# Optimization experiments

Hardware: AMD Instinct MI355X
Metric: run time of the kernel (lower is better)

## Reference

```python
import jax, jax.numpy as jnp
import numpy as np

B, L, D, H, M = 2, 4096, 1024, 16, 256
DH = D // H
EPS = 1e-6
LN_EPS = 1e-5


def setup_inputs() -> dict:
    key = jax.random.key(0)
    ks = jax.random.split(key, 6)
    inp = {
        "x": jax.random.normal(ks[0], (B, L, D), jnp.float32),
        "Wq": jax.random.normal(ks[1], (D, D), jnp.float32) * (D ** -0.5),
        "Wk": jax.random.normal(ks[2], (D, D), jnp.float32) * (D ** -0.5),
        "Wv": jax.random.normal(ks[3], (D, D), jnp.float32) * (D ** -0.5),
        "Wo": jax.random.normal(ks[4], (D, D), jnp.float32) * (D ** -0.5),
        "proj": jax.random.normal(ks[5], (H, M, DH), jnp.float32),
        "ln_g": jnp.ones((D,), jnp.float32),
        "ln_b": jnp.zeros((D,), jnp.float32),
        "scale_factor": 2,
    }
    return inp


def _heads(t, W):
    b, l, _ = t.shape
    return (t @ W).reshape(b, l, H, DH).transpose(0, 2, 1, 3)  # bhld


def _favor_features(u, proj):
    # u: [B,H,L,DH] already scaled by d_head**-0.25; proj: [H,M,DH]
    dash = jnp.einsum("bhld,hmd->bhlm", u, proj)
    diag = 0.5 * jnp.sum(u * u, axis=-1, keepdims=True)  # [B,H,L,1]
    stab = jnp.max(dash, axis=-1, keepdims=True)
    return jnp.exp(dash - diag - stab) * (M ** -0.5)  # [B,H,L,M]


def reference(x, Wq, Wk, Wv, Wo, proj, ln_g, ln_b, scale_factor):
    b, l, d = x.shape
    # nearest-neighbor upsample along sequence (F.interpolate default mode)
    up = jnp.repeat(x, scale_factor, axis=1)  # [B, L*s, D]

    scale = DH ** -0.25
    q = _heads(up, Wq) * scale   # [B,H,Lq,DH]
    k = _heads(x, Wk) * scale    # [B,H,L,DH]
    v = _heads(x, Wv)            # [B,H,L,DH]

    qf = _favor_features(q, proj)  # [B,H,Lq,M]
    kf = _favor_features(k, proj)  # [B,H,L,M]

    kv = jnp.einsum("bhlm,bhld->bhmd", kf, v)          # [B,H,M,DH]
    k_sum = jnp.sum(kf, axis=2)                          # [B,H,M]
    z = 1.0 / (jnp.einsum("bhlm,bhm->bhl", qf, k_sum) + EPS)
    attn = jnp.einsum("bhlm,bhmd->bhld", qf, kv) * z[..., None]

    lq = attn.shape[2]
    y = attn.transpose(0, 2, 1, 3).reshape(b, lq, d) @ Wo
    y = jax.nn.gelu(y, approximate=False)

    mu = jnp.mean(y, axis=-1, keepdims=True)
    var = jnp.mean((y - mu) ** 2, axis=-1, keepdims=True)
    return (y - mu) * jax.lax.rsqrt(var + LN_EPS) * ln_g + ln_b
```

## Files before the change

kernel.cpp:

```cpp
#include <hip/hip_runtime.h>

static constexpr int kB  = 2;
static constexpr int kL  = 4096;
static constexpr int kD  = 1024;
static constexpr int kH  = 16;
static constexpr int kDH = 64;
static constexpr int kM  = 256;
static constexpr int kN  = kB * kL;
static constexpr float kScale    = 0.35355339059327373f;
static constexpr float kInvSqrtM = 0.0625f;
static constexpr float kEps   = 1e-6f;
static constexpr float kLnEps = 1e-5f;

typedef __attribute__((ext_vector_type(8))) short short8;
typedef __attribute__((ext_vector_type(4))) float f32x4;

__device__ __forceinline__ float bf2f(unsigned short h) {
  union { unsigned int u; float f; } c;
  c.u = ((unsigned int)h) << 16;
  return c.f;
}
__device__ __forceinline__ unsigned short f2bf(float f) {
  union { float f; unsigned int u; } c;
  c.f = f;
  unsigned int u = c.u;
  u += 0x7fffu + ((u >> 16) & 1u);
  return (unsigned short)(u >> 16);
}

__device__ __forceinline__ void gload_lds16(const unsigned short* g,
                                            unsigned short* l) {
  __builtin_amdgcn_global_load_lds(
      (const __attribute__((address_space(1))) unsigned int*)g,
      (__attribute__((address_space(3))) unsigned int*)l, 16, 0, 0);
}

__device__ __forceinline__ void xcd_swizzle(int& bx, int& by) {
  const int nwg = gridDim.x * gridDim.y;
  const int bid = blockIdx.x + gridDim.x * blockIdx.y;
  const int cpx = nwg >> 3;
  const int sb  = (bid & 7) * cpx + (bid >> 3);
  bx = sb % gridDim.x;
  by = sb / gridDim.x;
}

__global__ __launch_bounds__(256) void cast_bf16_kernel(
    const float* __restrict__ in, unsigned short* __restrict__ out)
{
  const int i = blockIdx.x * 256 + threadIdx.x;
  float4 v = ((const float4*)in)[i];
  ushort4 o;
  o.x = f2bf(v.x); o.y = f2bf(v.y); o.z = f2bf(v.z); o.w = f2bf(v.w);
  ((ushort4*)out)[i] = o;
}

__global__ __launch_bounds__(256) void transpose_cast4_kernel(
    const float* __restrict__ W0, const float* __restrict__ W1,
    const float* __restrict__ W2, const float* __restrict__ W3,
    unsigned short* __restrict__ WqkvT, unsigned short* __restrict__ WoT)
{
  __shared__ float tile[32][33];
  const int z = blockIdx.z;
  const float* W = (z == 0) ? W0 : (z == 1) ? W1 : (z == 2) ? W2 : W3;
  unsigned short* WT = (z < 3) ? (WqkvT + (size_t)z * kD * kD) : WoT;
  const int n0 = blockIdx.x * 32, k0 = blockIdx.y * 32;
  const int t = threadIdx.x, kk = t >> 5, nn = t & 31;
#pragma unroll
  for (int i = 0; i < 4; ++i)
    tile[kk + i * 8][nn] = W[(size_t)(k0 + kk + i * 8) * kD + n0 + nn];
  __syncthreads();
#pragma unroll
  for (int i = 0; i < 4; ++i)
    WT[(size_t)(n0 + kk + i * 8) * kD + k0 + nn] = f2bf(tile[nn][kk + i * 8]);
}

#define GEMM_BK64_BODY(Aptr, Bptr, arow0, bcol0)                              \
  const int lrow = lane >> 3;                                                 \
  const int lcol = ((lane & 7) ^ lrow) * 8;        \
  f32x4 acc[4][4];                                                            \
  _Pragma("unroll")                                                           \
  for (int i = 0; i < 4; ++i)                                                 \
    _Pragma("unroll")                                                         \
    for (int j = 0; j < 4; ++j) acc[i][j] = (f32x4)0.f;                       \
  for (int k0 = 0; k0 < kD; k0 += 64) {                                       \
    _Pragma("unroll")                                                         \
    for (int i = 0; i < 4; ++i) {                                             \
      const int r0 = w * 32 + i * 8;                                          \
      gload_lds16(&Aptr[(size_t)(arow0 + r0 + lrow) * kD + k0 + lcol],        \
                  &As[r0 * 64]);                                              \
      gload_lds16(&Bptr[(size_t)(bcol0 + r0 + lrow) * kD + k0 + lcol],        \
                  &Bs[r0 * 64]);                                              \
    }                                                                         \
    __syncthreads();                                                          \
    _Pragma("unroll")                                                         \
    for (int ks = 0; ks < 2; ++ks) {                                          \
      short8 av[4], bv[4];                                                    \
      const int ch = ks * 4 + q;                                              \
      _Pragma("unroll")                                                       \
      for (int i = 0; i < 4; ++i)                                             \
        av[i] = *(const short8*)&As[(wr + i * 16 + c) * 64 +                  \
                                    ((ch ^ (c & 7)) * 8)];                    \
      _Pragma("unroll")                                                       \
      for (int j = 0; j < 4; ++j)                                             \
        bv[j] = *(const short8*)&Bs[(wc + j * 16 + c) * 64 +                  \
                                    ((ch ^ (c & 7)) * 8)];                    \
      _Pragma("unroll")                                                       \
      for (int i = 0; i < 4; ++i)                                             \
        _Pragma("unroll")                                                     \
        for (int j = 0; j < 4; ++j)                                           \
          acc[i][j] = __builtin_amdgcn_mfma_f32_16x16x32_bf16(                \
              av[i], bv[j], acc[i][j], 0, 0, 0);                              \
    }                                                                         \
    __syncthreads();                                                          \
  }

__global__ __launch_bounds__(256) void gemm_qk_mfma(
    const unsigned short* __restrict__ A, const unsigned short* __restrict__ BT,
    unsigned short* __restrict__ Qb, unsigned short* __restrict__ Kb)
{
  __shared__ unsigned short As[128 * 64];
  __shared__ unsigned short Bs[128 * 64];
  const int tid = threadIdx.x, lane = tid & 63, w = tid >> 6;
  const int q = lane >> 4, c = lane & 15;
  const int wr = (w >> 1) * 64, wc = (w & 1) * 64;
  int bx, by; xcd_swizzle(bx, by);
  const int row0 = by * 128, col0 = bx * 128;

  GEMM_BK64_BODY(A, BT, row0, col0)

  unsigned short* O = (col0 < 1024) ? Qb : Kb;
  const int cl0 = col0 & 1023;
#pragma unroll
  for (int i = 0; i < 4; ++i)
#pragma unroll
    for (int j = 0; j < 4; ++j)
#pragma unroll
      for (int r = 0; r < 4; ++r) {
        const int row = row0 + wr + i * 16 + q * 4 + r;
        const int col = cl0 + wc + j * 16 + c;
        O[(size_t)row * kD + col] = f2bf(kScale * acc[i][j][r]);
      }
}

__global__ __launch_bounds__(256) void gemm_vt_mfma(
    const unsigned short* __restrict__ A, const unsigned short* __restrict__ BT,
    unsigned short* __restrict__ VT)
{
  __shared__ unsigned short As[128 * 64];
  __shared__ unsigned short Bs[128 * 64];
  const int tid = threadIdx.x, lane = tid & 63, w = tid >> 6;
  const int q = lane >> 4, c = lane & 15;
  const int wr = (w >> 1) * 64, wc = (w & 1) * 64;
  int bx, by; xcd_swizzle(bx, by);
  const int row0 = bx * 128, col0 = by * 128;

  GEMM_BK64_BODY(A, BT, row0, col0)

#pragma unroll
  for (int i = 0; i < 4; ++i)
#pragma unroll
    for (int j = 0; j < 4; ++j)
#pragma unroll
      for (int r = 0; r < 4; ++r) {
        const int row = row0 + wr + i * 16 + q * 4 + r;
        const int col = col0 + wc + j * 16 + c;
        const int bq = col >> 12, l = col & 4095;
        const int h = row >> 6, d = row & 63;
        VT[((size_t)((bq * 16 + h) * 64 + d)) * (size_t)kL + l] =
            f2bf(acc[i][j][r]);
      }
}

__global__ __launch_bounds__(256) void gemm_wo_mfma(
    const unsigned short* __restrict__ A, const unsigned short* __restrict__ BT,
    unsigned short* __restrict__ Yb)
{
  __shared__ unsigned short As[128 * 64];
  __shared__ unsigned short Bs[128 * 64];
  const int tid = threadIdx.x, lane = tid & 63, w = tid >> 6;
  const int q = lane >> 4, c = lane & 15;
  const int wr = (w >> 1) * 64, wc = (w & 1) * 64;
  int bx, by; xcd_swizzle(bx, by);
  const int row0 = by * 128, col0 = bx * 128;

  GEMM_BK64_BODY(A, BT, row0, col0)

#pragma unroll
  for (int i = 0; i < 4; ++i)
#pragma unroll
    for (int j = 0; j < 4; ++j)
#pragma unroll
      for (int r = 0; r < 4; ++r) {
        const int row = row0 + wr + i * 16 + q * 4 + r;
        const int col = col0 + wc + j * 16 + c;
        Yb[(size_t)row * kD + col] = f2bf(acc[i][j][r]);
      }
}

__global__ __launch_bounds__(256) void favor_k_mfma(
    const unsigned short* __restrict__ U, const unsigned short* __restrict__ projb,
    unsigned short* __restrict__ F)
{
  __shared__ unsigned short Us[128 * 72];
  __shared__ unsigned short Ps[256 * 72];
  __shared__ float diagp[256];
  __shared__ float diag[128];
  unsigned short* Tbuf = Us;
  const int bh = blockIdx.x, b = bh >> 4, h = bh & 15;
  const int l0 = blockIdx.y * 128;
  const int tid = threadIdx.x, lane = tid & 63, w = tid >> 6;
  const int q = lane >> 4, c = lane & 15;
  const int wr = w * 32;

#pragma unroll
  for (int it = 0; it < 4; ++it) {
    int idx = it * 256 + tid;
    int row = idx >> 3, col8 = idx & 7;
    *(uint4*)&Us[row * 72 + col8 * 8] =
        *(const uint4*)&U[((size_t)(b * kL + l0 + row)) * kD + h * kDH + col8 * 8];
  }
#pragma unroll
  for (int it = 0; it < 8; ++it) {
    int idx = it * 256 + tid;
    int row = idx >> 3, col8 = idx & 7;
    *(uint4*)&Ps[row * 72 + col8 * 8] =
        *(const uint4*)&projb[((size_t)(h * kM + row)) * kDH + col8 * 8];
  }
  __syncthreads();

  {
    int row = tid & 127, half = tid >> 7;
    const unsigned short* ur = &Us[row * 72 + half * 32];
    float s = 0.f;
#pragma unroll
    for (int d8 = 0; d8 < 4; ++d8) {
      uint4 raw = *(const uint4*)&ur[d8 * 8];
      const unsigned short* us = (const unsigned short*)&raw;
#pragma unroll
      for (int j = 0; j < 8; ++j) { float v = bf2f(us[j]); s = fmaf(v, v, s); }
    }
    diagp[half * 128 + row] = s;
  }

  f32x4 acc[2][16];
#pragma unroll
  for (int i = 0; i < 2; ++i)
#pragma unroll
    for (int j = 0; j < 16; ++j) acc[i][j] = (f32x4)0.f;

#pragma unroll
  for (int ks = 0; ks < 2; ++ks) {
    short8 av[2];
#pragma unroll
    for (int i = 0; i < 2; ++i)
      av[i] = *(const short8*)&Us[(wr + i * 16 + c) * 72 + ks * 32 + q * 8];
#pragma unroll
    for (int jb = 0; jb < 2; ++jb) {
      short8 bv[8];
#pragma unroll
      for (int jl = 0; jl < 8; ++jl)
        bv[jl] = *(const short8*)&Ps[((jb * 8 + jl) * 16 + c) * 72 + ks * 32 + q * 8];
#pragma unroll
      for (int jl = 0; jl < 8; ++jl)
#pragma unroll
        for (int i = 0; i < 2; ++i)
          acc[i][jb * 8 + jl] = __builtin_amdgcn_mfma_f32_16x16x32_bf16(
              av[i], bv[jl], acc[i][jb * 8 + jl], 0, 0, 0);
    }
  }

  __syncthreads();
  if (tid < 128) diag[tid] = 0.5f * (diagp[tid] + diagp[128 + tid]);
  __syncthreads();

#pragma unroll
  for (int i = 0; i < 2; ++i)
#pragma unroll
    for (int r = 0; r < 4; ++r) {
      const int lrow = wr + i * 16 + q * 4 + r;
      float mx = -3.4e38f;
#pragma unroll
      for (int j = 0; j < 16; ++j) mx = fmaxf(mx, acc[i][j][r]);
      mx = fmaxf(mx, __shfl_xor(mx, 1, 64));
      mx = fmaxf(mx, __shfl_xor(mx, 2, 64));
      mx = fmaxf(mx, __shfl_xor(mx, 4, 64));
      mx = fmaxf(mx, __shfl_xor(mx, 8, 64));
      const float base = diag[lrow] + mx;
#pragma unroll
      for (int j = 0; j < 16; ++j)
        acc[i][j][r] = __expf(acc[i][j][r] - base) * kInvSqrtM;
    }

#pragma unroll
  for (int mc = 0; mc < 4; ++mc) {
    __syncthreads();
#pragma unroll
    for (int jl = 0; jl < 4; ++jl) {
      const int jj = mc * 4 + jl;
#pragma unroll
      for (int i = 0; i < 2; ++i) {
        ushort4 o;
        o.x = f2bf(acc[i][jj][0]); o.y = f2bf(acc[i][jj][1]);
        o.z = f2bf(acc[i][jj][2]); o.w = f2bf(acc[i][jj][3]);
        *(ushort4*)&Tbuf[(jl * 16 + c) * 136 + wr + i * 16 + q * 4] = o;
      }
    }
    __syncthreads();
#pragma unroll
    for (int it = 0; it < 4; ++it) {
      int idx = it * 256 + tid;
      int row = idx >> 4, col8 = idx & 15;
      *(uint4*)&F[((size_t)(bh * kM + mc * 64 + row)) * (size_t)kL +
                  l0 + col8 * 8] = *(const uint4*)&Tbuf[row * 136 + col8 * 8];
    }
  }
}

__global__ __launch_bounds__(256) void fused_qf_attn(
    const unsigned short* __restrict__ U, const unsigned short* __restrict__ projb,
    const unsigned short* __restrict__ KVT, unsigned short* __restrict__ ATTN)
{
  __shared__ unsigned short SA[22016];
  __shared__ float diagp[256];
  __shared__ float diag[128];
  __shared__ unsigned short ksumS[256];
  unsigned short* Us  = SA;
  unsigned short* Ps2 = SA + 9216;
  unsigned short* kvs = SA;
  unsigned short* qs  = SA + 16896;
  const int bh = blockIdx.x, b = bh >> 4, h = bh & 15;
  const int l0 = blockIdx.y * 128;
  const int tid = threadIdx.x, lane = tid & 63, w = tid >> 6;
  const int q = lane >> 4, c = lane & 15;
  const int wr = w * 32;

#pragma unroll
  for (int it = 0; it < 4; ++it) {
    int idx = it * 256 + tid;
    int row = idx >> 3, col8 = idx & 7;
    *(uint4*)&Us[row * 72 + col8 * 8] =
        *(const uint4*)&U[((size_t)(b * kL + l0 + row)) * kD + h * kDH + col8 * 8];
  }
#pragma unroll
  for (int it = 0; it < 4; ++it) {
    int idx = it * 256 + tid;
    int row = idx >> 3, col8 = idx & 7;
    *(uint4*)&Ps2[row * 72 + col8 * 8] =
        *(const uint4*)&projb[((size_t)(h * kM + row)) * kDH + col8 * 8];
  }
  __syncthreads();

  {
    int row = tid & 127, half = tid >> 7;
    const unsigned short* ur = &Us[row * 72 + half * 32];
    float s = 0.f;
#pragma unroll
    for (int d8 = 0; d8 < 4; ++d8) {
      uint4 raw = *(const uint4*)&ur[d8 * 8];
      const unsigned short* us = (const unsigned short*)&raw;
#pragma unroll
      for (int j = 0; j < 8; ++j) { float v = bf2f(us[j]); s = fmaf(v, v, s); }
    }
    diagp[half * 128 + row] = s;
  }

  f32x4 acc[2][16];
#pragma unroll
  for (int i = 0; i < 2; ++i)
#pragma unroll
    for (int j = 0; j < 16; ++j) acc[i][j] = (f32x4)0.f;

#pragma unroll
  for (int half = 0; half < 2; ++half) {
    if (half == 1) {
      __syncthreads();
#pragma unroll
      for (int it = 0; it < 4; ++it) {
        int idx = it * 256 + tid;
        int row = idx >> 3, col8 = idx & 7;
        *(uint4*)&Ps2[row * 72 + col8 * 8] =
            *(const uint4*)&projb[((size_t)(h * kM + 128 + row)) * kDH + col8 * 8];
      }
      __syncthreads();
    }
#pragma unroll
    for (int ks = 0; ks < 2; ++ks) {
      short8 av[2];
#pragma unroll
      for (int i = 0; i < 2; ++i)
        av[i] = *(const short8*)&Us[(wr + i * 16 + c) * 72 + ks * 32 + q * 8];
      short8 bv[8];
#pragma unroll
      for (int jl = 0; jl < 8; ++jl)
        bv[jl] = *(const short8*)&Ps2[(jl * 16 + c) * 72 + ks * 32 + q * 8];
#pragma unroll
      for (int jl = 0; jl < 8; ++jl)
#pragma unroll
        for (int i = 0; i < 2; ++i)
          acc[i][half * 8 + jl] = __builtin_amdgcn_mfma_f32_16x16x32_bf16(
              av[i], bv[jl], acc[i][half * 8 + jl], 0, 0, 0);
    }
  }

  __syncthreads();
  if (tid < 128) diag[tid] = 0.5f * (diagp[tid] + diagp[128 + tid]);
#pragma unroll
  for (int it = 0; it < 8; ++it) {
    int idx = it * 256 + tid;
    int row = idx >> 5, col8 = (idx & 31) * 8;
    *(uint4*)&kvs[row * 264 + col8] =
        *(const uint4*)&KVT[(size_t)bh * (80 * kM) + row * kM + col8];
  }
  if (tid < 32)
    *(uint4*)&ksumS[tid * 8] =
        *(const uint4*)&KVT[(size_t)bh * (80 * kM) + 64 * kM + tid * 8];
  __syncthreads();

#pragma unroll
  for (int i = 0; i < 2; ++i)
#pragma unroll
    for (int r = 0; r < 4; ++r) {
      const int lrow = wr + i * 16 + q * 4 + r;
      float mx = -3.4e38f;
#pragma unroll
      for (int j = 0; j < 16; ++j) mx = fmaxf(mx, acc[i][j][r]);
      mx = fmaxf(mx, __shfl_xor(mx, 1, 64));
      mx = fmaxf(mx, __shfl_xor(mx, 2, 64));
      mx = fmaxf(mx, __shfl_xor(mx, 4, 64));
      mx = fmaxf(mx, __shfl_xor(mx, 8, 64));
      const float base = diag[lrow] + mx;
#pragma unroll
      for (int j = 0; j < 16; ++j)
        acc[i][j][r] = __expf(acc[i][j][r] - base) * kInvSqrtM;
    }

  float z_[2][4];
#pragma unroll
  for (int i = 0; i < 2; ++i)
#pragma unroll
    for (int r = 0; r < 4; ++r) {
      float d = 0.f;
#pragma unroll
      for (int j = 0; j < 16; ++j)
        d = fmaf(acc[i][j][r], bf2f(ksumS[j * 16 + c]), d);
      d += __shfl_xor(d, 1, 64);
      d += __shfl_xor(d, 2, 64);
      d += __shfl_xor(d, 4, 64);
      d += __shfl_xor(d, 8, 64);
      z_[i][r] = 1.f / (d + kEps);
    }

  f32x4 acc2[2][4];
#pragma unroll
  for (int i = 0; i < 2; ++i)
#pragma unroll
    for (int j = 0; j < 4; ++j) acc2[i][j] = (f32x4)0.f;

#pragma unroll
  for (int kk = 0; kk < 8; ++kk) {
#pragma unroll
    for (int i = 0; i < 2; ++i)
#pragma unroll
      for (int jj2 = 0; jj2 < 2; ++jj2) {
        const int jj = kk * 2 + jj2;
#pragma unroll
        for (int r = 0; r < 4; ++r)
          qs[(wr + i * 16 + q * 4 + r) * 40 + jj2 * 16 + c] =
              f2bf(acc[i][jj][r]);
      }
    __syncthreads();
    short8 bv2[4];
#pragma unroll
    for (int j = 0; j < 4; ++j)
      bv2[j] = *(const short8*)&kvs[(j * 16 + c) * 264 + kk * 32 + q * 8];
#pragma unroll
    for (int i = 0; i < 2; ++i) {
      short8 av2 = *(const short8*)&qs[(w * 32 + i * 16 + c) * 40 + q * 8];
#pragma unroll
      for (int j = 0; j < 4; ++j)
        acc2[i][j] = __builtin_amdgcn_mfma_f32_16x16x32_bf16(
            av2, bv2[j], acc2[i][j], 0, 0, 0);
    }
    __syncthreads();
  }

#pragma unroll
  for (int i = 0; i < 2; ++i)
#pragma unroll
    for (int r = 0; r < 4; ++r) {
      const int row = l0 + w * 32 + i * 16 + q * 4 + r;
      const size_t base = ((size_t)(b * kL + row)) * kD + h * kDH;
#pragma unroll
      for (int j = 0; j < 4; ++j)
        ATTN[base + j * 16 + c] = f2bf(acc2[i][j][r] * z_[i][r]);
    }
}

__global__ __launch_bounds__(256) void kv_mfma(
    const unsigned short* __restrict__ KFT, const unsigned short* __restrict__ VT,
    float* __restrict__ KVP, float* __restrict__ KSP)
{
  __shared__ unsigned short As[128 * 32];
  __shared__ unsigned short Bs[64 * 32];
  const int bh = blockIdx.x, mtile = blockIdx.y, split = blockIdx.z;
  const int tid = threadIdx.x, lane = tid & 63, w = tid >> 6;
  const int q = lane >> 4, c = lane & 15;
  const int l0 = split * 512;
  const unsigned short* Abase = KFT + ((size_t)(bh * kM + mtile * 128)) * kL + l0;
  const unsigned short* Bbase = VT + ((size_t)(bh * kDH)) * kL + l0;
  const int lrow = lane >> 2, lcol = (lane & 3) * 8;

  f32x4 acc[2][4];
#pragma unroll
  for (int i = 0; i < 2; ++i)
#pragma unroll
    for (int j = 0; j < 4; ++j) acc[i][j] = (f32x4)0.f;
  float ksr[2] = {0.f, 0.f};

  for (int k0 = 0; k0 < 512; k0 += 32) {
#pragma unroll
    for (int i = 0; i < 2; ++i) {
      const int r0 = w * 32 + i * 16;
      gload_lds16(&Abase[(size_t)(r0 + lrow) * kL + k0 + lcol], &As[r0 * 32]);
    }
    gload_lds16(&Bbase[(size_t)(w * 16 + lrow) * kL + k0 + lcol], &Bs[w * 16 * 32]);
    __syncthreads();
    short8 av[2], bv[4];
#pragma unroll
    for (int i = 0; i < 2; ++i) {
      av[i] = *(const short8*)&As[(w * 32 + i * 16 + c) * 32 + q * 8];
#pragma unroll
      for (int e = 0; e < 8; ++e) ksr[i] += bf2f((unsigned short)av[i][e]);
    }
#pragma unroll
    for (int j = 0; j < 4; ++j)
      bv[j] = *(const short8*)&Bs[(j * 16 + c) * 32 + q * 8];
#pragma unroll
    for (int i = 0; i < 2; ++i)
#pragma unroll
      for (int j = 0; j < 4; ++j)
        acc[i][j] = __builtin_amdgcn_mfma_f32_16x16x32_bf16(
            av[i], bv[j], acc[i][j], 0, 0, 0);
    __syncthreads();
  }

  const int blk = (bh * 2 + mtile) * 8 + split;
  float* op = KVP + (size_t)blk * (128 * 64);
#pragma unroll
  for (int i = 0; i < 2; ++i)
#pragma unroll
    for (int j = 0; j < 4; ++j)
#pragma unroll
      for (int r = 0; r < 4; ++r)
        op[(w * 32 + i * 16 + q * 4 + r) * 64 + j * 16 + c] = acc[i][j][r];

#pragma unroll
  for (int i = 0; i < 2; ++i) {
    float s = ksr[i];
    s += __shfl_xor(s, 16, 64);
    s += __shfl_xor(s, 32, 64);
    if (q == 0) KSP[blk * 128 + w * 32 + i * 16 + c] = s;
  }
}

__global__ __launch_bounds__(256) void kv_reduce_kernel(
    const float* __restrict__ KVP, const float* __restrict__ KSP,
    unsigned short* __restrict__ KVT)
{
  const int blk = blockIdx.x;
  const int bh = blk / 80, n = blk - bh * 80;
  const int t = threadIdx.x;
  const int mt = t >> 7, ml = t & 127;
  float s = 0.f;
  if (n < 64) {
#pragma unroll
    for (int sp = 0; sp < 8; ++sp)
      s += KVP[((size_t)((bh * 2 + mt) * 8 + sp)) * (128 * 64) + ml * 64 + n];
  } else if (n == 64) {
#pragma unroll
    for (int sp = 0; sp < 8; ++sp)
      s += KSP[((bh * 2 + mt) * 8 + sp) * 128 + ml];
  }
  KVT[(size_t)bh * (80 * kM) + n * kM + t] = f2bf(s);
}

__global__ __launch_bounds__(256) void gelu_ln_kernel(
    const unsigned short* __restrict__ Yb, const float* __restrict__ lng,
    const float* __restrict__ lnb, float* __restrict__ OUT)
{
  __shared__ float r1[4], r2[4];
  const int n = blockIdx.x;
  const int tid = threadIdx.x, lane = tid & 63, w = tid >> 6;

  ushort4 yv = ((const ushort4*)(Yb + (size_t)n * kD))[tid];
  float y0 = bf2f(yv.x), y1 = bf2f(yv.y), y2 = bf2f(yv.z), y3 = bf2f(yv.w);
  float g0 = 0.5f * y0 * (1.f + erff(y0 * 0.70710678118654752f));
  float g1 = 0.5f * y1 * (1.f + erff(y1 * 0.70710678118654752f));
  float g2 = 0.5f * y2 * (1.f + erff(y2 * 0.70710678118654752f));
  float g3 = 0.5f * y3 * (1.f + erff(y3 * 0.70710678118654752f));

  float s  = (g0 + g1) + (g2 + g3);
  float ss = (g0 * g0 + g1 * g1) + (g2 * g2 + g3 * g3);
#pragma unroll
  for (int off = 32; off; off >>= 1) {
    s  += __shfl_xor(s, off, 64);
    ss += __shfl_xor(ss, off, 64);
  }
  if (lane == 0) { r1[w] = s; r2[w] = ss; }
  __syncthreads();
  s  = (r1[0] + r1[1]) + (r1[2] + r1[3]);
  ss = (r2[0] + r2[1]) + (r2[2] + r2[3]);
  float mu  = s * (1.f / (float)kD);
  float var = ss * (1.f / (float)kD) - mu * mu;
  float inv = rsqrtf(var + kLnEps);

  float4 gg = ((const float4*)lng)[tid];
  float4 bb = ((const float4*)lnb)[tid];
  float4 o;
  o.x = (g0 - mu) * inv * gg.x + bb.x;
  o.y = (g1 - mu) * inv * gg.y + bb.y;
  o.z = (g2 - mu) * inv * gg.z + bb.z;
  o.w = (g3 - mu) * inv * gg.w + bb.w;

  const int b = n >> 12, l = n & 4095;
  const int cc = tid * 4;
  size_t base = ((size_t)(b * 8192 + 2 * l)) * kD + cc;
  *(float4*)(OUT + base)      = o;
  *(float4*)(OUT + base + kD) = o;
}

extern "C" void kernel_launch(void* const* d_in, const int* in_sizes, int n_in,
                              void* d_out, int out_size, void* d_ws, size_t ws_size,
                              hipStream_t stream)
{
  (void)in_sizes; (void)n_in; (void)out_size; (void)ws_size;
  const float* x    = (const float*)d_in[0];
  const float* Wq   = (const float*)d_in[1];
  const float* Wk   = (const float*)d_in[2];
  const float* Wv   = (const float*)d_in[3];
  const float* Wo   = (const float*)d_in[4];
  const float* proj = (const float*)d_in[5];
  const float* lng  = (const float*)d_in[6];
  const float* lnb  = (const float*)d_in[7];
  float* out = (float*)d_out;

  char* ws = (char*)d_ws;
  const size_t MB = 1024 * 1024;
  unsigned short* xb    = (unsigned short*)(ws);
  unsigned short* WqkvT = (unsigned short*)(ws + 16 * MB);
  unsigned short* WoT   = (unsigned short*)(ws + 22 * MB);
  unsigned short* Qb    = (unsigned short*)(ws + 24 * MB);
  unsigned short* Kb    = (unsigned short*)(ws + 40 * MB);
  unsigned short* VT    = (unsigned short*)(ws + 56 * MB);
  float* KVP            = (float*)(ws + 72 * MB);
  unsigned short* KFT   = (unsigned short*)(ws + 136 * MB);
  float* KSP            = (float*)(ws + 200 * MB);
  unsigned short* KVT   = (unsigned short*)(ws + 201 * MB);
  unsigned short* projb = (unsigned short*)(ws + 203 * MB);
  unsigned short* ATTN  = Kb;
  unsigned short* Yb    = (unsigned short*)(ws + 72 * MB);
  unsigned short* WvT   = WqkvT + (size_t)2 * kD * kD;

  cast_bf16_kernel<<<(kN * kD) / 1024, 256, 0, stream>>>(x, xb);
  cast_bf16_kernel<<<(kH * kM * kDH) / 1024, 256, 0, stream>>>(proj, projb);
  transpose_cast4_kernel<<<dim3(32, 32, 4), 256, 0, stream>>>(
      Wq, Wk, Wv, Wo, WqkvT, WoT);

  gemm_qk_mfma<<<dim3(16, 64), 256, 0, stream>>>(xb, WqkvT, Qb, Kb);
  gemm_vt_mfma<<<dim3(8, 64), 256, 0, stream>>>(WvT, xb, VT);

  favor_k_mfma<<<dim3(32, 32), 256, 0, stream>>>(Kb, projb, KFT);
  kv_mfma<<<dim3(32, 2, 8), 256, 0, stream>>>(KFT, VT, KVP, KSP);
  kv_reduce_kernel<<<32 * 80, 256, 0, stream>>>(KVP, KSP, KVT);

  fused_qf_attn<<<dim3(32, 32), 256, 0, stream>>>(Qb, projb, KVT, ATTN);

  gemm_wo_mfma<<<dim3(8, 64), 256, 0, stream>>>(ATTN, WoT, Yb);

  gelu_ln_kernel<<<kN, 256, 0, stream>>>(Yb, lng, lnb, out);
}
```

Before: 329.1 us.

## Merge QK and V projection GEMMs into one launch; widen kv_mfma K-tile to 64

The separate Q/K and V^T projection GEMMs are combined into a single launch of 24x64 blocks. Blocks with bx>=16 compute the V^T tile by swapping operands, which removes one launch and its tail. Separately, kv_mfma now stages 64-wide K chunks with an XOR swizzle on the LDS layout. That halves its loop iterations and barriers and is meant to reduce LDS bank conflicts. In exchange it doubles shared memory per block, and the xcd_swizzle mapping over the larger grid may change cache locality.

```diff
diff --git a/kernel.cpp b/kernel.cpp
--- a/kernel.cpp
+++ b/kernel.cpp
@@ -114,9 +114,10 @@
     __syncthreads();                                                          \
   }
 
-__global__ __launch_bounds__(256) void gemm_qk_mfma(
-    const unsigned short* __restrict__ A, const unsigned short* __restrict__ BT,
-    unsigned short* __restrict__ Qb, unsigned short* __restrict__ Kb)
+__global__ __launch_bounds__(256) void gemm_qkv_mfma(
+    const unsigned short* __restrict__ xb, const unsigned short* __restrict__ WqkvT,
+    unsigned short* __restrict__ Qb, unsigned short* __restrict__ Kb,
+    unsigned short* __restrict__ VT)
 {
   __shared__ unsigned short As[128 * 64];
   __shared__ unsigned short Bs[128 * 64];
@@ -124,51 +125,43 @@
   const int q = lane >> 4, c = lane & 15;
   const int wr = (w >> 1) * 64, wc = (w & 1) * 64;
   int bx, by; xcd_swizzle(bx, by);
-  const int row0 = by * 128, col0 = bx * 128;
-
-  GEMM_BK64_BODY(A, BT, row0, col0)
-
-  unsigned short* O = (col0 < 1024) ? Qb : Kb;
-  const int cl0 = col0 & 1023;
-#pragma unroll
-  for (int i = 0; i < 4; ++i)
-#pragma unroll
-    for (int j = 0; j < 4; ++j)
-#pragma unroll
-      for (int r = 0; r < 4; ++r) {
-        const int row = row0 + wr + i * 16 + q * 4 + r;
-        const int col = cl0 + wc + j * 16 + c;
-        O[(size_t)row * kD + col] = f2bf(kScale * acc[i][j][r]);
-      }
-}
-
-__global__ __launch_bounds__(256) void gemm_vt_mfma(
-    const unsigned short* __restrict__ A, const unsigned short* __restrict__ BT,
-    unsigned short* __restrict__ VT)
-{
-  __shared__ unsigned short As[128 * 64];
-  __shared__ unsigned short Bs[128 * 64];
-  const int tid = threadIdx.x, lane = tid & 63, w = tid >> 6;
-  const int q = lane >> 4, c = lane & 15;
-  const int wr = (w >> 1) * 64, wc = (w & 1) * 64;
-  int bx, by; xcd_swizzle(bx, by);
-  const int row0 = bx * 128, col0 = by * 128;
-
-  GEMM_BK64_BODY(A, BT, row0, col0)
-
-#pragma unroll
-  for (int i = 0; i < 4; ++i)
-#pragma unroll
-    for (int j = 0; j < 4; ++j)
-#pragma unroll
-      for (int r = 0; r < 4; ++r) {
-        const int row = row0 + wr + i * 16 + q * 4 + r;
-        const int col = col0 + wc + j * 16 + c;
-        const int bq = col >> 12, l = col & 4095;
-        const int h = row >> 6, d = row & 63;
-        VT[((size_t)((bq * 16 + h) * 64 + d)) * (size_t)kL + l] =
-            f2bf(acc[i][j][r]);
-      }
+  const bool isv = (bx >= 16);
+  const unsigned short* WvT = WqkvT + (size_t)2 * kD * kD;
+  const unsigned short* Ap = isv ? WvT : xb;
+  const unsigned short* Bp = isv ? xb : WqkvT;
+  const int arow0 = isv ? (bx - 16) * 128 : by * 128;
+  const int bcol0 = isv ? by * 128 : bx * 128;
+
+  GEMM_BK64_BODY(Ap, Bp, arow0, bcol0)
+
+  if (!isv) {
+    unsigned short* O = (bcol0 < 1024) ? Qb : Kb;
+    const int cl0 = bcol0 & 1023;
+#pragma unroll
+    for (int i = 0; i < 4; ++i)
+#pragma unroll
+      for (int j = 0; j < 4; ++j)
+#pragma unroll
+        for (int r = 0; r < 4; ++r) {
+          const int row = arow0 + wr + i * 16 + q * 4 + r;
+          const int col = cl0 + wc + j * 16 + c;
+          O[(size_t)row * kD + col] = f2bf(kScale * acc[i][j][r]);
+        }
+  } else {
+#pragma unroll
+    for (int i = 0; i < 4; ++i)
+#pragma unroll
+      for (int j = 0; j < 4; ++j)
+#pragma unroll
+        for (int r = 0; r < 4; ++r) {
+          const int row = arow0 + wr + i * 16 + q * 4 + r;
+          const int col = bcol0 + wc + j * 16 + c;
+          const int bq = col >> 12, l = col & 4095;
+          const int h = row >> 6, d = row & 63;
+          VT[((size_t)((bq * 16 + h) * 64 + d)) * (size_t)kL + l] =
+              f2bf(acc[i][j][r]);
+        }
+  }
 }
 
 __global__ __launch_bounds__(256) void gemm_wo_mfma(
@@ -500,15 +493,16 @@
     const unsigned short* __restrict__ KFT, const unsigned short* __restrict__ VT,
     float* __restrict__ KVP, float* __restrict__ KSP)
 {
-  __shared__ unsigned short As[128 * 32];
-  __shared__ unsigned short Bs[64 * 32];
+  __shared__ unsigned short As[128 * 64];
+  __shared__ unsigned short Bs[64 * 64];
   const int bh = blockIdx.x, mtile = blockIdx.y, split = blockIdx.z;
   const int tid = threadIdx.x, lane = tid & 63, w = tid >> 6;
   const int q = lane >> 4, c = lane & 15;
   const int l0 = split * 512;
   const unsigned short* Abase = KFT + ((size_t)(bh * kM + mtile * 128)) * kL + l0;
   const unsigned short* Bbase = VT + ((size_t)(bh * kDH)) * kL + l0;
-  const int lrow = lane >> 2, lcol = (lane & 3) * 8;
+  const int lrow = lane >> 3;
+  const int lcol = ((lane & 7) ^ lrow) * 8;
 
   f32x4 acc[2][4];
 #pragma unroll
@@ -517,30 +511,39 @@
     for (int j = 0; j < 4; ++j) acc[i][j] = (f32x4)0.f;
   float ksr[2] = {0.f, 0.f};
 
-  for (int k0 = 0; k0 < 512; k0 += 32) {
+  for (int k0 = 0; k0 < 512; k0 += 64) {
+#pragma unroll
+    for (int i = 0; i < 4; ++i) {
+      const int r0 = w * 32 + i * 8;
+      gload_lds16(&Abase[(size_t)(r0 + lrow) * kL + k0 + lcol], &As[r0 * 64]);
+    }
 #pragma unroll
     for (int i = 0; i < 2; ++i) {
-      const int r0 = w * 32 + i * 16;
-      gload_lds16(&Abase[(size_t)(r0 + lrow) * kL + k0 + lcol], &As[r0 * 32]);
-    }
-    gload_lds16(&Bbase[(size_t)(w * 16 + lrow) * kL + k0 + lcol], &Bs[w * 16 * 32]);
+      const int r0 = w * 16 + i * 8;
+      gload_lds16(&Bbase[(size_t)(r0 + lrow) * kL + k0 + lcol], &Bs[r0 * 64]);
+    }
     __syncthreads();
-    short8 av[2], bv[4];
-#pragma unroll
-    for (int i = 0; i < 2; ++i) {
-      av[i] = *(const short8*)&As[(w * 32 + i * 16 + c) * 32 + q * 8];
-#pragma unroll
-      for (int e = 0; e < 8; ++e) ksr[i] += bf2f((unsigned short)av[i][e]);
-    }
-#pragma unroll
-    for (int j = 0; j < 4; ++j)
-      bv[j] = *(const short8*)&Bs[(j * 16 + c) * 32 + q * 8];
-#pragma unroll
-    for (int i = 0; i < 2; ++i)
+#pragma unroll
+    for (int ks = 0; ks < 2; ++ks) {
+      short8 av[2], bv[4];
+      const int ch = ks * 4 + q;
+#pragma unroll
+      for (int i = 0; i < 2; ++i) {
+        av[i] = *(const short8*)&As[(w * 32 + i * 16 + c) * 64 +
+                                    ((ch ^ (c & 7)) * 8)];
+#pragma unroll
+        for (int e = 0; e < 8; ++e) ksr[i] += bf2f((unsigned short)av[i][e]);
+      }
 #pragma unroll
       for (int j = 0; j < 4; ++j)
-        acc[i][j] = __builtin_amdgcn_mfma_f32_16x16x32_bf16(
-            av[i], bv[j], acc[i][j], 0, 0, 0);
+        bv[j] = *(const short8*)&Bs[(j * 16 + c) * 64 + ((ch ^ (c & 7)) * 8)];
+#pragma unroll
+      for (int i = 0; i < 2; ++i)
+#pragma unroll
+        for (int j = 0; j < 4; ++j)
+          acc[i][j] = __builtin_amdgcn_mfma_f32_16x16x32_bf16(
+              av[i], bv[j], acc[i][j], 0, 0, 0);
+    }
     __syncthreads();
   }
 
@@ -659,15 +662,13 @@
   unsigned short* projb = (unsigned short*)(ws + 203 * MB);
   unsigned short* ATTN  = Kb;
   unsigned short* Yb    = (unsigned short*)(ws + 72 * MB);
-  unsigned short* WvT   = WqkvT + (size_t)2 * kD * kD;
 
   cast_bf16_kernel<<<(kN * kD) / 1024, 256, 0, stream>>>(x, xb);
   cast_bf16_kernel<<<(kH * kM * kDH) / 1024, 256, 0, stream>>>(proj, projb);
   transpose_cast4_kernel<<<dim3(32, 32, 4), 256, 0, stream>>>(
       Wq, Wk, Wv, Wo, WqkvT, WoT);
 
-  gemm_qk_mfma<<<dim3(16, 64), 256, 0, stream>>>(xb, WqkvT, Qb, Kb);
-  gemm_vt_mfma<<<dim3(8, 64), 256, 0, stream>>>(WvT, xb, VT);
+  gemm_qkv_mfma<<<dim3(24, 64), 256, 0, stream>>>(xb, WqkvT, Qb, Kb, VT);
 
   favor_k_mfma<<<dim3(32, 32), 256, 0, stream>>>(Kb, projb, KFT);
   kv_mfma<<<dim3(32, 2, 8), 256, 0, stream>>>(KFT, VT, KVP, KSP);
```

Measured after the change: 324.7 us. No clear change (-1.3%).
